# Performance work log

Hardware: AMD Instinct MI355X
Metric: run time of the kernel (lower is better)

Reference implementation:

```python
import jax, jax.numpy as jnp
import numpy as np

ADAPTER_RATIO = 0.2


def setup_inputs() -> dict:
    key = jax.random.key(0)
    k1, k2, k3, k4, k5 = jax.random.split(key, 5)
    B, C, H, D = 16384, 512, 128, 3  # batch, feature dim, bottleneck, n_domains
    n_text = (D + 1) * 345           # original + 3 domain prompt sets, 345 classes
    return {
        "image_features": jax.random.normal(k1, (B, C), dtype=jnp.float32),
        "domain_label": jax.random.randint(k2, (B,), 0, D),
        "W1": jax.random.normal(k3, (D, C, H), dtype=jnp.float32) * 0.02,
        "W2": jax.random.normal(k4, (D, H, C), dtype=jnp.float32) * 0.02,
        "text_features": jax.random.normal(k5, (n_text, C), dtype=jnp.float32),
        "logit_scale": jnp.ones((1,), dtype=jnp.float32) * jnp.log(jnp.float32(100.0)),
    }


def reference(image_features, domain_label, W1, W2, text_features, logit_scale):
    # Per-sample routed adapters: run all D tiny adapters densely, then gather
    # each sample's routed output (equivalent to torch per-sample dispatch loop).
    h = jax.nn.relu(jnp.einsum("bi,dij->dbj", image_features, W1))   # [D,B,H]
    a = jax.nn.relu(jnp.einsum("dbj,djk->dbk", h, W2))                # [D,B,C]
    adapter_features = jnp.take_along_axis(
        a, domain_label[None, :, None], axis=0)[0]                     # [B,C]
    feats = ADAPTER_RATIO * adapter_features + (1.0 - ADAPTER_RATIO) * image_features
    feats = feats / jnp.linalg.norm(feats, axis=-1, keepdims=True)
    # text features are pre-normalized in the original module
    txt = text_features / jnp.linalg.norm(text_features, axis=-1, keepdims=True)
    logits = jnp.exp(logit_scale[0]) * (feats @ txt.T)                 # [B, n_text]
    return logits
```

## Files before the change

kernel.cpp:

```cpp
#include <hip/hip_runtime.h>
#include <math.h>

typedef __bf16 bf16;
typedef __attribute__((ext_vector_type(8))) __bf16 bf16x8;
typedef __attribute__((ext_vector_type(4))) __bf16 bf16x4;
typedef __attribute__((ext_vector_type(4))) float f32x4;

#define MFMA(a, b, c) __builtin_amdgcn_mfma_f32_16x16x32_bf16((a), (b), (c), 0, 0, 0)
#define BARR() __builtin_amdgcn_s_barrier()
#define SFEN() __builtin_amdgcn_sched_barrier(0)
#define WAITV(n) asm volatile("s_waitcnt vmcnt(" #n ")" ::: "memory")

static constexpr int NB = 16384;
static constexpr int NC = 512;
static constexpr int NH = 128;
static constexpr int ND = 3;
static constexpr int NT = 1380;
static constexpr int NTP = 1408;
static constexpr int NTILE = 131;
static constexpr int NPMAX = NTILE * 128;

__device__ __forceinline__ void gld16(const bf16* g, void* l) {
  __builtin_amdgcn_global_load_lds(
      (const __attribute__((address_space(1))) void*)g,
      (__attribute__((address_space(3))) void*)l, 16, 0, 0);
}

__global__ __launch_bounds__(64) void k_prep(
    const float* __restrict__ X, const float* __restrict__ W1,
    const float* __restrict__ W2, const float* __restrict__ txt,
    bf16* __restrict__ Xbf, bf16* __restrict__ W1t,
    bf16* __restrict__ W2t, bf16* __restrict__ Tbf)
{
  __shared__ float tl[64][65];
  const int b = blockIdx.x, t = threadIdx.x;
  if (b < NTP) {
    bf16x4* dst = (bf16x4*)(Tbf + (size_t)b * NC);
    if (b < NT) {
      const float4* src = (const float4*)(txt + (size_t)b * NC);
      float4 u0 = src[t * 2], u1 = src[t * 2 + 1];
      float ssq = u0.x * u0.x + u0.y * u0.y + u0.z * u0.z + u0.w * u0.w +
                  u1.x * u1.x + u1.y * u1.y + u1.z * u1.z + u1.w * u1.w;
      for (int m = 32; m; m >>= 1) ssq += __shfl_xor(ssq, m, 64);
      float inv = 1.0f / sqrtf(ssq);
      bf16x4 o0 = {(bf16)(u0.x * inv), (bf16)(u0.y * inv), (bf16)(u0.z * inv), (bf16)(u0.w * inv)};
      bf16x4 o1 = {(bf16)(u1.x * inv), (bf16)(u1.y * inv), (bf16)(u1.z * inv), (bf16)(u1.w * inv)};
      dst[t * 2] = o0; dst[t * 2 + 1] = o1;
    } else {
      bf16x4 z = {(bf16)0.f, (bf16)0.f, (bf16)0.f, (bf16)0.f};
      dst[t * 2] = z; dst[t * 2 + 1] = z;
    }
  } else if (b < NTP + 48) {
    const int e = b - NTP, d = e >> 4, rem = e & 15;
    const int i0 = (rem >> 1) * 64, n0 = (rem & 1) * 64;
    const float* src = W1 + (size_t)d * NC * NH;
    for (int r = 0; r < 64; ++r) tl[r][t] = src[(size_t)(i0 + r) * NH + n0 + t];
    __syncthreads();
    bf16* dst = W1t + (size_t)d * NH * NC;
    for (int r = 0; r < 64; ++r)
      dst[(size_t)(n0 + r) * NC + i0 + t] = (bf16)tl[t][r];
  } else if (b < NTP + 96) {
    const int e = b - (NTP + 48), d = e >> 4, rem = e & 15;
    const int j0 = (rem >> 3) * 64, n0 = (rem & 7) * 64;
    const float* src = W2 + (size_t)d * NH * NC;
    for (int r = 0; r < 64; ++r) tl[r][t] = src[(size_t)(j0 + r) * NC + n0 + t];
    __syncthreads();
    bf16* dst = W2t + (size_t)d * NC * NH;
    for (int r = 0; r < 64; ++r)
      dst[(size_t)(n0 + r) * NH + j0 + t] = (bf16)tl[t][r];
  } else {
    const int id = b - (NTP + 96);
    const float4* src = (const float4*)X;
    bf16x4* dst = (bf16x4*)Xbf;
    const size_t base = (size_t)id * 1024 + (size_t)t * 16;
    for (int i = 0; i < 16; ++i) {
      float4 u = src[base + i];
      bf16x4 o = {(bf16)u.x, (bf16)u.y, (bf16)u.z, (bf16)u.w};
      dst[base + i] = o;
    }
  }
}

__global__ __launch_bounds__(1024) void k_sort(
    const int* __restrict__ lab, int* __restrict__ map, int* __restrict__ dmeta)
{
  __shared__ int woff[16][3];
  __shared__ int segbase[4];
  __shared__ int padded[3];
  const int t = threadIdx.x, lane = t & 63, wv = t >> 6;
  int c[3] = {0, 0, 0};
  int ld[16];
  const int base = t * 16;
#pragma unroll
  for (int i = 0; i < 16; ++i) { ld[i] = lab[base + i]; c[ld[i]]++; }
  int exc[3];
#pragma unroll
  for (int d = 0; d < 3; ++d) {
    int v = c[d];
    for (int off = 1; off < 64; off <<= 1) {
      int u = __shfl_up(v, off, 64);
      if (lane >= off) v += u;
    }
    exc[d] = v - c[d];
    if (lane == 63) woff[wv][d] = v;
  }
  __syncthreads();
  if (t == 0) {
    int tot[3] = {0, 0, 0};
    for (int w = 0; w < 16; ++w)
      for (int d = 0; d < 3; ++d) { int v = woff[w][d]; woff[w][d] = tot[d]; tot[d] += v; }
    int s = 0;
    for (int d = 0; d < 3; ++d) {
      padded[d] = (tot[d] + 127) & ~127;
      segbase[d] = s; s += padded[d];
    }
    segbase[3] = s;
    dmeta[NTILE] = s;
  }
  __syncthreads();
  for (int tile = t; tile < NTILE; tile += 1024) {
    const int slot = tile * 128;
    int dd = -1;
    for (int d = 0; d < 3; ++d)
      if (slot >= segbase[d] && slot < segbase[d] + padded[d]) dd = d;
    dmeta[tile] = dd;
  }
  for (int i = t; i < NPMAX; i += 1024) map[i] = -1;
  __syncthreads();
  int pos[3];
#pragma unroll
  for (int d = 0; d < 3; ++d) pos[d] = segbase[d] + woff[wv][d] + exc[d];
#pragma unroll
  for (int i = 0; i < 16; ++i) { int d = ld[i]; map[pos[d]++] = base + i; }
}

__global__ __launch_bounds__(512) void k_adapter(
    const bf16* __restrict__ Xbf, const bf16* __restrict__ W1t,
    const bf16* __restrict__ W2t, const int* __restrict__ map,
    const int* __restrict__ dmeta, bf16* __restrict__ Fbf)
{
  __shared__ bf16 As[2][64 * 64];
  __shared__ bf16 Hs[64 * 128];
  __shared__ float rssq[8][64];
  __shared__ int smap[64];
  const int bx = blockIdx.x;
  const int d = dmeta[bx >> 1];
  if (d < 0) return;
  const int t = threadIdx.x, w = t >> 6, l = t & 63;
  const int lr = l & 15, lg = l >> 4;
  const int row0 = bx * 64;
  if (t < 64) smap[t] = map[row0 + t];

  int arow = map[row0 + (t >> 3)]; if (arow < 0) arow = 0;
  const int scolb = ((t & 7) * 16) ^ (((t >> 3) & 7) << 4);
#define STGA(buf, kt)                                                        \
  gld16(Xbf + (size_t)arow * NC + (kt) * 64 + (scolb >> 1),                  \
        (char*)As[buf] + t * 16);

  f32x4 acc1[4] = {};
  const bf16* W1B = W1t + (size_t)d * NH * NC + (size_t)(w * 16 + lr) * NC;
  STGA(0, 0); STGA(1, 1);
#pragma unroll 1
  for (int kt = 0; kt < 8; ++kt) {
    const int cur = kt & 1;
    if (kt == 7) { WAITV(0); } else { WAITV(1); }
    BARR(); SFEN();
#pragma unroll
    for (int h = 0; h < 2; ++h) {
      bf16x8 a[4];
#pragma unroll
      for (int m = 0; m < 4; ++m) {
        const int r = m * 16 + lr;
        a[m] = *(const bf16x8*)((const char*)As[cur] +
                                r * 128 + ((h * 64 + lg * 16) ^ ((r & 7) << 4)));
      }
      const bf16x8 bq = *(const bf16x8*)(W1B + kt * 64 + h * 32 + lg * 8);
#pragma unroll
      for (int m = 0; m < 4; ++m) acc1[m] = MFMA(a[m], bq, acc1[m]);
    }
    BARR(); SFEN();
    if (kt + 2 < 8) STGA(cur, kt + 2);
  }
#undef STGA

#pragma unroll
  for (int m = 0; m < 4; ++m)
#pragma unroll
    for (int r = 0; r < 4; ++r) {
      const int row = m * 16 + lg * 4 + r;
      const int colb = (w * 16 + lr) * 2;
      const float v = acc1[m][r];
      *(bf16*)((char*)Hs + row * 256 + (colb ^ ((row & 7) << 4))) =
          (bf16)(v > 0.f ? v : 0.f);
    }
  __syncthreads();

  f32x4 acc[4][4] = {};
  const bf16* W2B = W2t + (size_t)d * NC * NH + (size_t)(w * 64) * NH;
#pragma unroll
  for (int ks = 0; ks < 4; ++ks) {
    bf16x8 a[4], bq[4];
#pragma unroll
    for (int m = 0; m < 4; ++m) {
      const int r = m * 16 + lr;
      a[m] = *(const bf16x8*)((const char*)Hs +
                              r * 256 + ((ks * 64 + lg * 16) ^ ((r & 7) << 4)));
    }
#pragma unroll
    for (int n = 0; n < 4; ++n)
      bq[n] = *(const bf16x8*)(W2B + (size_t)(n * 16 + lr) * NH + ks * 32 + lg * 8);
#pragma unroll
    for (int m = 0; m < 4; ++m)
#pragma unroll
      for (int n = 0; n < 4; ++n)
        acc[m][n] = MFMA(a[m], bq[n], acc[m][n]);
  }

  const int col0 = w * 64;
#pragma unroll
  for (int m = 0; m < 4; ++m)
#pragma unroll
    for (int r = 0; r < 4; ++r) {
      const int rl = m * 16 + lg * 4 + r;
      const int grow = smap[rl];
      const size_t row = grow < 0 ? 0 : (size_t)grow;
      float part = 0.f;
#pragma unroll
      for (int n = 0; n < 4; ++n) {
        const int col = col0 + n * 16 + lr;
        float v = acc[m][n][r];
        v = v > 0.f ? v : 0.f;
        v = 0.2f * v + 0.8f * (float)Xbf[row * NC + col];
        acc[m][n][r] = v;
        part += v * v;
      }
      part += __shfl_xor(part, 1, 64);
      part += __shfl_xor(part, 2, 64);
      part += __shfl_xor(part, 4, 64);
      part += __shfl_xor(part, 8, 64);
      if (lr == 0) rssq[w][rl] = part;
    }
  __syncthreads();
#pragma unroll
  for (int m = 0; m < 4; ++m)
#pragma unroll
    for (int r = 0; r < 4; ++r) {
      const int rl = m * 16 + lg * 4 + r;
      const int grow = smap[rl];
      if (grow < 0) continue;
      float tot = 0.f;
#pragma unroll
      for (int ww = 0; ww < 8; ++ww) tot += rssq[ww][rl];
      const float inv = 1.0f / sqrtf(tot);
#pragma unroll
      for (int n = 0; n < 4; ++n) {
        const int col = col0 + n * 16 + lr;
        Fbf[(size_t)grow * NC + col] = (bf16)(acc[m][n][r] * inv);
      }
    }
}

__global__ __launch_bounds__(256) void k_gemm3(
    const bf16* __restrict__ Fbf, const bf16* __restrict__ Tbf,
    const float* __restrict__ lsc, float* __restrict__ out)
{
  __shared__ bf16 As[2][128 * 32];
  __shared__ bf16 Bs[2][128 * 32];
  const int bx = blockIdx.x, by = blockIdx.y;
  const int t = threadIdx.x, w = t >> 6, l = t & 63;
  const int wr = w >> 1, wc = w & 1;
  const int lr = l & 15, lg = l >> 4;
  const int row0 = bx * 128, col0 = by * 128;
  const bf16* Ag = Fbf + (size_t)row0 * NC;
  const bf16* Bg = Tbf + (size_t)col0 * NC;

#define STG3(buf, kt)                                                         \
  {                                                                           \
    _Pragma("unroll")                                                         \
    for (int i = 0; i < 2; ++i) {                                             \
      const int off = (i * 256 + t) * 16;                                     \
      const int row = off >> 6;                                               \
      const int src = (off & 63) ^ (((row >> 1) & 3) << 4);                   \
      const size_t go = (size_t)row * NC + (size_t)(kt) * 32 + (src >> 1);    \
      gld16(Ag + go, (char*)As[buf] + off);                                   \
      gld16(Bg + go, (char*)Bs[buf] + off);                                   \
    }                                                                         \
  }

  f32x4 acc[4][4] = {};
  STG3(0, 0);
#pragma unroll 1
  for (int ks = 0; ks < 16; ++ks) {
    const int cur = ks & 1;
    __syncthreads();
    if (ks + 1 < 16) STG3(cur ^ 1, ks + 1);
    bf16x8 a[4], b[4];
#pragma unroll
    for (int m = 0; m < 4; ++m) {
      const int r = wr * 64 + m * 16 + lr;
      a[m] = *(const bf16x8*)&As[cur][r * 32 + ((lg * 8) ^ (((r >> 1) & 3) << 3))];
    }
#pragma unroll
    for (int n = 0; n < 4; ++n) {
      const int r = wc * 64 + n * 16 + lr;
      b[n] = *(const bf16x8*)&Bs[cur][r * 32 + ((lg * 8) ^ (((r >> 1) & 3) << 3))];
    }
#pragma unroll
    for (int m = 0; m < 4; ++m)
#pragma unroll
      for (int n = 0; n < 4; ++n)
        acc[m][n] = MFMA(a[m], b[n], acc[m][n]);
  }

  const float s = expf(lsc[0]);
#pragma unroll
  for (int m = 0; m < 4; ++m)
#pragma unroll
    for (int n = 0; n < 4; ++n)
#pragma unroll
      for (int r = 0; r < 4; ++r) {
        const int row = row0 + wr * 64 + m * 16 + lg * 4 + r;
        const int col = col0 + wc * 64 + n * 16 + lr;
        if (col < NT) out[(size_t)row * NT + col] = s * acc[m][n][r];
      }
#undef STG3
}

extern "C" void kernel_launch(void* const* d_in, const int* in_sizes, int n_in,
                              void* d_out, int out_size, void* d_ws, size_t ws_size,
                              hipStream_t stream) {
  const float* X   = (const float*)d_in[0];
  const int*   lab = (const int*)d_in[1];
  const float* W1  = (const float*)d_in[2];
  const float* W2  = (const float*)d_in[3];
  const float* txt = (const float*)d_in[4];
  const float* lsc = (const float*)d_in[5];
  float* out = (float*)d_out;

  char* ws = (char*)d_ws;
  constexpr size_t SZ_XBF = (size_t)NB * NC * 2;
  constexpr size_t SZ_W1T = (size_t)ND * NH * NC * 2;
  constexpr size_t SZ_W2T = (size_t)ND * NC * NH * 2;
  constexpr size_t SZ_TBF = (size_t)NTP * NC * 2;
  constexpr size_t SZ_FBF = (size_t)NB * NC * 2;
  constexpr size_t SZ_MAP = (size_t)NPMAX * 4;
  bf16* Xbf = (bf16*)(ws);
  bf16* W1t = (bf16*)(ws + SZ_XBF);
  bf16* W2t = (bf16*)(ws + SZ_XBF + SZ_W1T);
  bf16* Tbf = (bf16*)(ws + SZ_XBF + SZ_W1T + SZ_W2T);
  bf16* Fbf = (bf16*)(ws + SZ_XBF + SZ_W1T + SZ_W2T + SZ_TBF);
  int*  map = (int*)(ws + SZ_XBF + SZ_W1T + SZ_W2T + SZ_TBF + SZ_FBF);
  int*  dmeta = (int*)(ws + SZ_XBF + SZ_W1T + SZ_W2T + SZ_TBF + SZ_FBF + SZ_MAP);

  k_prep<<<NTP + 96 + 2048, 64, 0, stream>>>(X, W1, W2, txt,
                                             Xbf, W1t, W2t, Tbf);
  k_sort<<<1, 1024, 0, stream>>>(lab, map, dmeta);
  k_adapter<<<2 * NTILE, 512, 0, stream>>>(Xbf, W1t, W2t, map, dmeta, Fbf);
  k_gemm3<<<dim3(NB / 128, NTP / 128), 256, 0, stream>>>(Fbf, Tbf, lsc, out);
}
```

Measured before the change: 97.62 us.

## Deepen final GEMM pipeline with BK=64 tiles and explicit waitcnt scheduling

The final logits GEMM now stages 64-wide K tiles (8 iterations instead of 16) with a new XOR swizzle over 128-byte rows. It prefetches two stages ahead, replacing __syncthreads with explicit vmcnt/lgkmcnt waits, and issues the next global-to-LDS loads between the two MFMA half-steps. MFMA sections also raise wave priority. This aims to hide global load latency and cut barrier overhead, at the cost of doubling LDS use to 64KB per block, which may lower occupancy.

```diff
diff --git a/kernel.cpp b/kernel.cpp
--- a/kernel.cpp
+++ b/kernel.cpp
@@ -10,6 +10,7 @@
 #define BARR() __builtin_amdgcn_s_barrier()
 #define SFEN() __builtin_amdgcn_sched_barrier(0)
 #define WAITV(n) asm volatile("s_waitcnt vmcnt(" #n ")" ::: "memory")
+#define LGKM0() asm volatile("s_waitcnt lgkmcnt(0)" ::: "memory")
 
 static constexpr int NB = 16384;
 static constexpr int NC = 512;
@@ -264,8 +265,8 @@
     const bf16* __restrict__ Fbf, const bf16* __restrict__ Tbf,
     const float* __restrict__ lsc, float* __restrict__ out)
 {
-  __shared__ bf16 As[2][128 * 32];
-  __shared__ bf16 Bs[2][128 * 32];
+  __shared__ bf16 As[2][128 * 64];
+  __shared__ bf16 Bs[2][128 * 64];
   const int bx = blockIdx.x, by = blockIdx.y;
   const int t = threadIdx.x, w = t >> 6, l = t & 63;
   const int wr = w >> 1, wc = w & 1;
@@ -274,42 +275,82 @@
   const bf16* Ag = Fbf + (size_t)row0 * NC;
   const bf16* Bg = Tbf + (size_t)col0 * NC;
 
+  int srow[4], scol[4];
+#pragma unroll
+  for (int i = 0; i < 4; ++i) {
+    const int off = (i * 256 + t) * 16;
+    srow[i] = off >> 7;
+    scol[i] = ((off & 127) ^ ((srow[i] & 7) << 4)) >> 1;
+  }
 #define STG3(buf, kt)                                                         \
   {                                                                           \
     _Pragma("unroll")                                                         \
-    for (int i = 0; i < 2; ++i) {                                             \
+    for (int i = 0; i < 4; ++i) {                                             \
       const int off = (i * 256 + t) * 16;                                     \
-      const int row = off >> 6;                                               \
-      const int src = (off & 63) ^ (((row >> 1) & 3) << 4);                   \
-      const size_t go = (size_t)row * NC + (size_t)(kt) * 32 + (src >> 1);    \
-      gld16(Ag + go, (char*)As[buf] + off);                                   \
-      gld16(Bg + go, (char*)Bs[buf] + off);                                   \
+      gld16(Ag + (size_t)srow[i] * NC + (kt) * 64 + scol[i],                  \
+            (char*)As[buf] + off);                                            \
     }                                                                         \
+    _Pragma("unroll")                                                         \
+    for (int i = 0; i < 4; ++i) {                                             \
+      const int off = (i * 256 + t) * 16;                                     \
+      gld16(Bg + (size_t)srow[i] * NC + (kt) * 64 + scol[i],                  \
+            (char*)Bs[buf] + off);                                            \
+    }                                                                         \
   }
 
   f32x4 acc[4][4] = {};
-  STG3(0, 0);
+  STG3(0, 0); STG3(1, 1);
 #pragma unroll 1
-  for (int ks = 0; ks < 16; ++ks) {
-    const int cur = ks & 1;
-    __syncthreads();
-    if (ks + 1 < 16) STG3(cur ^ 1, ks + 1);
-    bf16x8 a[4], b[4];
-#pragma unroll
-    for (int m = 0; m < 4; ++m) {
-      const int r = wr * 64 + m * 16 + lr;
-      a[m] = *(const bf16x8*)&As[cur][r * 32 + ((lg * 8) ^ (((r >> 1) & 3) << 3))];
-    }
-#pragma unroll
-    for (int n = 0; n < 4; ++n) {
-      const int r = wc * 64 + n * 16 + lr;
-      b[n] = *(const bf16x8*)&Bs[cur][r * 32 + ((lg * 8) ^ (((r >> 1) & 3) << 3))];
-    }
-#pragma unroll
-    for (int m = 0; m < 4; ++m)
-#pragma unroll
-      for (int n = 0; n < 4; ++n)
-        acc[m][n] = MFMA(a[m], b[n], acc[m][n]);
+  for (int k = 0; k < 8; ++k) {
+    const int c = k & 1;
+    if (k < 7) { WAITV(8); } else { WAITV(0); }
+    BARR(); SFEN();
+    const char* Ab = (const char*)As[c];
+    const char* Bb = (const char*)Bs[c];
+    {
+      bf16x8 a[4], b[4];
+#pragma unroll
+      for (int m = 0; m < 4; ++m) {
+        const int r = wr * 64 + m * 16 + lr;
+        a[m] = *(const bf16x8*)(Ab + r * 128 + ((lg * 16) ^ ((r & 7) << 4)));
+      }
+#pragma unroll
+      for (int n = 0; n < 4; ++n) {
+        const int r = wc * 64 + n * 16 + lr;
+        b[n] = *(const bf16x8*)(Bb + r * 128 + ((lg * 16) ^ ((r & 7) << 4)));
+      }
+      LGKM0(); SFEN();
+      __builtin_amdgcn_s_setprio(1);
+#pragma unroll
+      for (int m = 0; m < 4; ++m)
+#pragma unroll
+        for (int n = 0; n < 4; ++n)
+          acc[m][n] = MFMA(a[m], b[n], acc[m][n]);
+      __builtin_amdgcn_s_setprio(0);
+    }
+    {
+      bf16x8 a[4], b[4];
+#pragma unroll
+      for (int m = 0; m < 4; ++m) {
+        const int r = wr * 64 + m * 16 + lr;
+        a[m] = *(const bf16x8*)(Ab + r * 128 + ((64 + lg * 16) ^ ((r & 7) << 4)));
+      }
+#pragma unroll
+      for (int n = 0; n < 4; ++n) {
+        const int r = wc * 64 + n * 16 + lr;
+        b[n] = *(const bf16x8*)(Bb + r * 128 + ((64 + lg * 16) ^ ((r & 7) << 4)));
+      }
+      LGKM0(); SFEN();
+      BARR(); SFEN();
+      if (k + 2 < 8) STG3(c, k + 2);
+      __builtin_amdgcn_s_setprio(1);
+#pragma unroll
+      for (int m = 0; m < 4; ++m)
+#pragma unroll
+        for (int n = 0; n < 4; ++n)
+          acc[m][n] = MFMA(a[m], b[n], acc[m][n]);
+      __builtin_amdgcn_s_setprio(0);
+    }
   }
 
   const float s = expf(lsc[0]);
```

New measurement: 97.22 us. About the same (-0.4%).

## Keep feature row tile resident in LDS and sweep all text columns per block

Applied to the files above, without the earlier changes.

The final logits GEMM now gives each 512-thread block a 64-row slice of normalized features, loads its full K=512 into LDS once, and loops over six 256-column text tiles. Only the text tiles are double-buffered, with explicit vmcnt waits, barriers and MFMA priority raising. This removes the repeated reloading of feature tiles across column blocks. The cost is more padding of text rows (1380 to 1536), fewer blocks (256), larger LDS use and serialized column tiles inside each block.

```diff
diff --git a/kernel.cpp b/kernel.cpp
--- a/kernel.cpp
+++ b/kernel.cpp
@@ -10,13 +10,14 @@
 #define BARR() __builtin_amdgcn_s_barrier()
 #define SFEN() __builtin_amdgcn_sched_barrier(0)
 #define WAITV(n) asm volatile("s_waitcnt vmcnt(" #n ")" ::: "memory")
+#define LGKM0() asm volatile("s_waitcnt lgkmcnt(0)" ::: "memory")
 
 static constexpr int NB = 16384;
 static constexpr int NC = 512;
 static constexpr int NH = 128;
 static constexpr int ND = 3;
 static constexpr int NT = 1380;
-static constexpr int NTP = 1408;
+static constexpr int NTPAD = 1536;
 static constexpr int NTILE = 131;
 static constexpr int NPMAX = NTILE * 128;
 
@@ -34,7 +35,7 @@
 {
   __shared__ float tl[64][65];
   const int b = blockIdx.x, t = threadIdx.x;
-  if (b < NTP) {
+  if (b < NTPAD) {
     bf16x4* dst = (bf16x4*)(Tbf + (size_t)b * NC);
     if (b < NT) {
       const float4* src = (const float4*)(txt + (size_t)b * NC);
@@ -50,8 +51,8 @@
       bf16x4 z = {(bf16)0.f, (bf16)0.f, (bf16)0.f, (bf16)0.f};
       dst[t * 2] = z; dst[t * 2 + 1] = z;
     }
-  } else if (b < NTP + 48) {
-    const int e = b - NTP, d = e >> 4, rem = e & 15;
+  } else if (b < NTPAD + 48) {
+    const int e = b - NTPAD, d = e >> 4, rem = e & 15;
     const int i0 = (rem >> 1) * 64, n0 = (rem & 1) * 64;
     const float* src = W1 + (size_t)d * NC * NH;
     for (int r = 0; r < 64; ++r) tl[r][t] = src[(size_t)(i0 + r) * NH + n0 + t];
@@ -59,8 +60,8 @@
     bf16* dst = W1t + (size_t)d * NH * NC;
     for (int r = 0; r < 64; ++r)
       dst[(size_t)(n0 + r) * NC + i0 + t] = (bf16)tl[t][r];
-  } else if (b < NTP + 96) {
-    const int e = b - (NTP + 48), d = e >> 4, rem = e & 15;
+  } else if (b < NTPAD + 96) {
+    const int e = b - (NTPAD + 48), d = e >> 4, rem = e & 15;
     const int j0 = (rem >> 3) * 64, n0 = (rem & 7) * 64;
     const float* src = W2 + (size_t)d * NH * NC;
     for (int r = 0; r < 64; ++r) tl[r][t] = src[(size_t)(j0 + r) * NC + n0 + t];
@@ -69,7 +70,7 @@
     for (int r = 0; r < 64; ++r)
       dst[(size_t)(n0 + r) * NH + j0 + t] = (bf16)tl[t][r];
   } else {
-    const int id = b - (NTP + 96);
+    const int id = b - (NTPAD + 96);
     const float4* src = (const float4*)X;
     bf16x4* dst = (bf16x4*)Xbf;
     const size_t base = (size_t)id * 1024 + (size_t)t * 16;
@@ -260,70 +261,85 @@
     }
 }
 
-__global__ __launch_bounds__(256) void k_gemm3(
+__global__ __launch_bounds__(512) void k_gemm3(
     const bf16* __restrict__ Fbf, const bf16* __restrict__ Tbf,
     const float* __restrict__ lsc, float* __restrict__ out)
 {
-  __shared__ bf16 As[2][128 * 32];
-  __shared__ bf16 Bs[2][128 * 32];
-  const int bx = blockIdx.x, by = blockIdx.y;
+  __shared__ bf16 Fs[64 * 512];
+  __shared__ bf16 Bs[2][256 * 32];
+  const int bx = blockIdx.x;
   const int t = threadIdx.x, w = t >> 6, l = t & 63;
-  const int wr = w >> 1, wc = w & 1;
+  const int wr = w >> 2, wc = w & 3;
   const int lr = l & 15, lg = l >> 4;
-  const int row0 = bx * 128, col0 = by * 128;
+  const int row0 = bx * 64;
   const bf16* Ag = Fbf + (size_t)row0 * NC;
-  const bf16* Bg = Tbf + (size_t)col0 * NC;
-
-#define STG3(buf, kt)                                                         \
+
+#pragma unroll
+  for (int i = 0; i < 8; ++i) {
+    const int off = (i * 512 + t) * 16;
+    const int row = off >> 10;
+    const int srcb = (off & 1023) ^ ((row & 7) << 4);
+    gld16(Ag + (size_t)row * NC + (srcb >> 1), (char*)Fs + off);
+  }
+#define STGB(buf, nt, kt)                                                     \
   {                                                                           \
     _Pragma("unroll")                                                         \
     for (int i = 0; i < 2; ++i) {                                             \
-      const int off = (i * 256 + t) * 16;                                     \
+      const int off = (i * 512 + t) * 16;                                     \
       const int row = off >> 6;                                               \
-      const int src = (off & 63) ^ (((row >> 1) & 3) << 4);                   \
-      const size_t go = (size_t)row * NC + (size_t)(kt) * 32 + (src >> 1);    \
-      gld16(Ag + go, (char*)As[buf] + off);                                   \
-      gld16(Bg + go, (char*)Bs[buf] + off);                                   \
+      const int srcb = (off & 63) ^ (((row >> 1) & 3) << 4);                  \
+      gld16(Tbf + (size_t)((nt) * 256 + row) * NC + (kt) * 32 + (srcb >> 1),  \
+            (char*)Bs[buf] + off);                                            \
     }                                                                         \
   }
 
-  f32x4 acc[4][4] = {};
-  STG3(0, 0);
+  const float s = expf(lsc[0]);
 #pragma unroll 1
-  for (int ks = 0; ks < 16; ++ks) {
-    const int cur = ks & 1;
-    __syncthreads();
-    if (ks + 1 < 16) STG3(cur ^ 1, ks + 1);
-    bf16x8 a[4], b[4];
-#pragma unroll
-    for (int m = 0; m < 4; ++m) {
-      const int r = wr * 64 + m * 16 + lr;
-      a[m] = *(const bf16x8*)&As[cur][r * 32 + ((lg * 8) ^ (((r >> 1) & 3) << 3))];
-    }
-#pragma unroll
-    for (int n = 0; n < 4; ++n) {
-      const int r = wc * 64 + n * 16 + lr;
-      b[n] = *(const bf16x8*)&Bs[cur][r * 32 + ((lg * 8) ^ (((r >> 1) & 3) << 3))];
-    }
-#pragma unroll
-    for (int m = 0; m < 4; ++m)
+  for (int nt = 0; nt < 6; ++nt) {
+    STGB(0, nt, 0); STGB(1, nt, 1);
+    f32x4 acc[2][4] = {};
+#pragma unroll 1
+    for (int kt = 0; kt < 16; ++kt) {
+      const int c = kt & 1;
+      if (kt < 15) { WAITV(2); } else { WAITV(0); }
+      BARR(); SFEN();
+      bf16x8 a[2], b[4];
+#pragma unroll
+      for (int m = 0; m < 2; ++m) {
+        const int r = wr * 32 + m * 16 + lr;
+        a[m] = *(const bf16x8*)((const char*)Fs + r * 1024 +
+                                ((kt * 64 + lg * 16) ^ ((r & 7) << 4)));
+      }
+#pragma unroll
+      for (int n = 0; n < 4; ++n) {
+        const int r = wc * 64 + n * 16 + lr;
+        b[n] = *(const bf16x8*)((const char*)Bs[c] + r * 64 +
+                                ((lg * 16) ^ (((r >> 1) & 3) << 4)));
+      }
+      LGKM0(); SFEN();
+      __builtin_amdgcn_s_setprio(1);
+#pragma unroll
+      for (int m = 0; m < 2; ++m)
+#pragma unroll
+        for (int n = 0; n < 4; ++n)
+          acc[m][n] = MFMA(a[m], b[n], acc[m][n]);
+      __builtin_amdgcn_s_setprio(0);
+      BARR(); SFEN();
+      if (kt + 2 < 16) STGB(c, nt, kt + 2);
+    }
+    const int col0 = nt * 256 + wc * 64;
+#pragma unroll
+    for (int m = 0; m < 2; ++m)
 #pragma unroll
       for (int n = 0; n < 4; ++n)
-        acc[m][n] = MFMA(a[m], b[n], acc[m][n]);
-  }
-
-  const float s = expf(lsc[0]);
-#pragma unroll
-  for (int m = 0; m < 4; ++m)
-#pragma unroll
-    for (int n = 0; n < 4; ++n)
-#pragma unroll
-      for (int r = 0; r < 4; ++r) {
-        const int row = row0 + wr * 64 + m * 16 + lg * 4 + r;
-        const int col = col0 + wc * 64 + n * 16 + lr;
-        if (col < NT) out[(size_t)row * NT + col] = s * acc[m][n][r];
-      }
-#undef STG3
+#pragma unroll
+        for (int r = 0; r < 4; ++r) {
+          const int row = row0 + wr * 32 + m * 16 + lg * 4 + r;
+          const int col = col0 + n * 16 + lr;
+          if (col < NT) out[(size_t)row * NT + col] = s * acc[m][n][r];
+        }
+  }
+#undef STGB
 }
 
 extern "C" void kernel_launch(void* const* d_in, const int* in_sizes, int n_in,
@@ -341,7 +357,7 @@
   constexpr size_t SZ_XBF = (size_t)NB * NC * 2;
   constexpr size_t SZ_W1T = (size_t)ND * NH * NC * 2;
   constexpr size_t SZ_W2T = (size_t)ND * NC * NH * 2;
-  constexpr size_t SZ_TBF = (size_t)NTP * NC * 2;
+  constexpr size_t SZ_TBF = (size_t)NTPAD * NC * 2;
   constexpr size_t SZ_FBF = (size_t)NB * NC * 2;
   constexpr size_t SZ_MAP = (size_t)NPMAX * 4;
   bf16* Xbf = (bf16*)(ws);
@@ -352,9 +368,9 @@
   int*  map = (int*)(ws + SZ_XBF + SZ_W1T + SZ_W2T + SZ_TBF + SZ_FBF);
   int*  dmeta = (int*)(ws + SZ_XBF + SZ_W1T + SZ_W2T + SZ_TBF + SZ_FBF + SZ_MAP);
 
-  k_prep<<<NTP + 96 + 2048, 64, 0, stream>>>(X, W1, W2, txt,
-                                             Xbf, W1t, W2t, Tbf);
+  k_prep<<<NTPAD + 96 + 2048, 64, 0, stream>>>(X, W1, W2, txt,
+                                               Xbf, W1t, W2t, Tbf);
   k_sort<<<1, 1024, 0, stream>>>(lab, map, dmeta);
   k_adapter<<<2 * NTILE, 512, 0, stream>>>(Xbf, W1t, W2t, map, dmeta, Fbf);
-  k_gemm3<<<dim3(NB / 128, NTP / 128), 256, 0, stream>>>(Fbf, Tbf, lsc, out);
-}
+  k_gemm3<<<NB / 64, 512, 0, stream>>>(Fbf, Tbf, lsc, out);
+}
```

New measurement: 125.2 us. +28.3%, slower.

## Fuse fp32-to-bf16 conversion of image features into adapter kernel loads

Applied to the files above, without the earlier changes.

Removes the separate X-to-bf16 conversion pass from the prep kernel and its workspace buffer. The adapter kernel now loads fp32 rows through registers, converts to bf16 and writes them into swizzled LDS, prefetching two steps ahead. The residual blend reads fp32 X directly, which also avoids bf16 rounding there. In exchange it saves a full write and read of the bf16 X copy, but replaces async global-to-LDS loads with register staging that adds VGPR pressure and LDS write latency inside the K loop.

```diff
diff --git a/kernel.cpp b/kernel.cpp
--- a/kernel.cpp
+++ b/kernel.cpp
@@ -10,6 +10,7 @@
 #define BARR() __builtin_amdgcn_s_barrier()
 #define SFEN() __builtin_amdgcn_sched_barrier(0)
 #define WAITV(n) asm volatile("s_waitcnt vmcnt(" #n ")" ::: "memory")
+#define LGKM0() asm volatile("s_waitcnt lgkmcnt(0)" ::: "memory")
 
 static constexpr int NB = 16384;
 static constexpr int NC = 512;
@@ -27,10 +28,9 @@
 }
 
 __global__ __launch_bounds__(64) void k_prep(
-    const float* __restrict__ X, const float* __restrict__ W1,
-    const float* __restrict__ W2, const float* __restrict__ txt,
-    bf16* __restrict__ Xbf, bf16* __restrict__ W1t,
-    bf16* __restrict__ W2t, bf16* __restrict__ Tbf)
+    const float* __restrict__ W1, const float* __restrict__ W2,
+    const float* __restrict__ txt,
+    bf16* __restrict__ W1t, bf16* __restrict__ W2t, bf16* __restrict__ Tbf)
 {
   __shared__ float tl[64][65];
   const int b = blockIdx.x, t = threadIdx.x;
@@ -59,7 +59,7 @@
     bf16* dst = W1t + (size_t)d * NH * NC;
     for (int r = 0; r < 64; ++r)
       dst[(size_t)(n0 + r) * NC + i0 + t] = (bf16)tl[t][r];
-  } else if (b < NTP + 96) {
+  } else {
     const int e = b - (NTP + 48), d = e >> 4, rem = e & 15;
     const int j0 = (rem >> 3) * 64, n0 = (rem & 7) * 64;
     const float* src = W2 + (size_t)d * NH * NC;
@@ -68,16 +68,6 @@
     bf16* dst = W2t + (size_t)d * NC * NH;
     for (int r = 0; r < 64; ++r)
       dst[(size_t)(n0 + r) * NH + j0 + t] = (bf16)tl[t][r];
-  } else {
-    const int id = b - (NTP + 96);
-    const float4* src = (const float4*)X;
-    bf16x4* dst = (bf16x4*)Xbf;
-    const size_t base = (size_t)id * 1024 + (size_t)t * 16;
-    for (int i = 0; i < 16; ++i) {
-      float4 u = src[base + i];
-      bf16x4 o = {(bf16)u.x, (bf16)u.y, (bf16)u.z, (bf16)u.w};
-      dst[base + i] = o;
-    }
   }
 }
 
@@ -135,7 +125,7 @@
 }
 
 __global__ __launch_bounds__(512) void k_adapter(
-    const bf16* __restrict__ Xbf, const bf16* __restrict__ W1t,
+    const float* __restrict__ X, const bf16* __restrict__ W1t,
     const bf16* __restrict__ W2t, const int* __restrict__ map,
     const int* __restrict__ dmeta, bf16* __restrict__ Fbf)
 {
@@ -152,19 +142,34 @@
   if (t < 64) smap[t] = map[row0 + t];
 
   int arow = map[row0 + (t >> 3)]; if (arow < 0) arow = 0;
-  const int scolb = ((t & 7) * 16) ^ (((t >> 3) & 7) << 4);
-#define STGA(buf, kt)                                                        \
-  gld16(Xbf + (size_t)arow * NC + (kt) * 64 + (scolb >> 1),                  \
-        (char*)As[buf] + t * 16);
+  const float4* Xr = (const float4*)(X + (size_t)arow * NC);
+  const int f4b = (t & 7) * 2;
+  const int wrow = t >> 3;
+  const int wcb = ((t & 7) * 16) ^ ((wrow & 7) << 4);
+
+  float4 R0a, R0b, R1a, R1b;
+#define LOADR0(kt) { R0a = Xr[(kt) * 16 + f4b]; R0b = Xr[(kt) * 16 + f4b + 1]; }
+#define LOADR1(kt) { R1a = Xr[(kt) * 16 + f4b]; R1b = Xr[(kt) * 16 + f4b + 1]; }
+#define CVTW(buf, Ra, Rb) {                                                   \
+    bf16x8 v_;                                                                \
+    v_[0] = (bf16)Ra.x; v_[1] = (bf16)Ra.y; v_[2] = (bf16)Ra.z;               \
+    v_[3] = (bf16)Ra.w; v_[4] = (bf16)Rb.x; v_[5] = (bf16)Rb.y;               \
+    v_[6] = (bf16)Rb.z; v_[7] = (bf16)Rb.w;                                   \
+    *(bf16x8*)((char*)As[buf] + wrow * 128 + wcb) = v_; }
 
   f32x4 acc1[4] = {};
   const bf16* W1B = W1t + (size_t)d * NH * NC + (size_t)(w * 16 + lr) * NC;
-  STGA(0, 0); STGA(1, 1);
+  LOADR0(0); LOADR1(1);
+  CVTW(0, R0a, R0b);
+  LOADR0(2);
+  LGKM0(); BARR(); SFEN();
 #pragma unroll 1
   for (int kt = 0; kt < 8; ++kt) {
     const int cur = kt & 1;
-    if (kt == 7) { WAITV(0); } else { WAITV(1); }
-    BARR(); SFEN();
+    if (kt + 1 < 8) {
+      if (cur == 0) { CVTW(1, R1a, R1b); if (kt + 3 < 8) LOADR1(kt + 3); }
+      else          { CVTW(0, R0a, R0b); if (kt + 3 < 8) LOADR0(kt + 3); }
+    }
 #pragma unroll
     for (int h = 0; h < 2; ++h) {
       bf16x8 a[4];
@@ -178,10 +183,11 @@
 #pragma unroll
       for (int m = 0; m < 4; ++m) acc1[m] = MFMA(a[m], bq, acc1[m]);
     }
-    BARR(); SFEN();
-    if (kt + 2 < 8) STGA(cur, kt + 2);
-  }
-#undef STGA
+    LGKM0(); SFEN(); BARR(); SFEN();
+  }
+#undef LOADR0
+#undef LOADR1
+#undef CVTW
 
 #pragma unroll
   for (int m = 0; m < 4; ++m)
@@ -230,7 +236,7 @@
         const int col = col0 + n * 16 + lr;
         float v = acc[m][n][r];
         v = v > 0.f ? v : 0.f;
-        v = 0.2f * v + 0.8f * (float)Xbf[row * NC + col];
+        v = 0.2f * v + 0.8f * X[row * NC + col];
         acc[m][n][r] = v;
         part += v * v;
       }
@@ -338,23 +344,20 @@
   float* out = (float*)d_out;
 
   char* ws = (char*)d_ws;
-  constexpr size_t SZ_XBF = (size_t)NB * NC * 2;
   constexpr size_t SZ_W1T = (size_t)ND * NH * NC * 2;
   constexpr size_t SZ_W2T = (size_t)ND * NC * NH * 2;
   constexpr size_t SZ_TBF = (size_t)NTP * NC * 2;
   constexpr size_t SZ_FBF = (size_t)NB * NC * 2;
   constexpr size_t SZ_MAP = (size_t)NPMAX * 4;
-  bf16* Xbf = (bf16*)(ws);
-  bf16* W1t = (bf16*)(ws + SZ_XBF);
-  bf16* W2t = (bf16*)(ws + SZ_XBF + SZ_W1T);
-  bf16* Tbf = (bf16*)(ws + SZ_XBF + SZ_W1T + SZ_W2T);
-  bf16* Fbf = (bf16*)(ws + SZ_XBF + SZ_W1T + SZ_W2T + SZ_TBF);
-  int*  map = (int*)(ws + SZ_XBF + SZ_W1T + SZ_W2T + SZ_TBF + SZ_FBF);
-  int*  dmeta = (int*)(ws + SZ_XBF + SZ_W1T + SZ_W2T + SZ_TBF + SZ_FBF + SZ_MAP);
-
-  k_prep<<<NTP + 96 + 2048, 64, 0, stream>>>(X, W1, W2, txt,
-                                             Xbf, W1t, W2t, Tbf);
+  bf16* W1t = (bf16*)(ws);
+  bf16* W2t = (bf16*)(ws + SZ_W1T);
+  bf16* Tbf = (bf16*)(ws + SZ_W1T + SZ_W2T);
+  bf16* Fbf = (bf16*)(ws + SZ_W1T + SZ_W2T + SZ_TBF);
+  int*  map = (int*)(ws + SZ_W1T + SZ_W2T + SZ_TBF + SZ_FBF);
+  int*  dmeta = (int*)(ws + SZ_W1T + SZ_W2T + SZ_TBF + SZ_FBF + SZ_MAP);
+
+  k_prep<<<NTP + 96, 64, 0, stream>>>(W1, W2, txt, W1t, W2t, Tbf);
   k_sort<<<1, 1024, 0, stream>>>(lab, map, dmeta);
-  k_adapter<<<2 * NTILE, 512, 0, stream>>>(Xbf, W1t, W2t, map, dmeta, Fbf);
+  k_adapter<<<2 * NTILE, 512, 0, stream>>>(X, W1t, W2t, map, dmeta, Fbf);
   k_gemm3<<<dim3(NB / 128, NTP / 128), 256, 0, stream>>>(Fbf, Tbf, lsc, out);
 }
```

New measurement: 92.75 us. 1.05x faster.
